# Performance work log

Measured on AMD Instinct MI355X. Metric: run time of the kernel, lower is better.

The kernel has to match this reference:

```python
import jax, jax.numpy as jnp
import numpy as np

D3D, D2D, DTEXT, DPROJ, SEQ_LEN = 256, 768, 3072, 3072, 256
B, S, T = 32, 256, 512


def setup_inputs() -> dict:
    key = jax.random.key(0)
    ks = jax.random.split(key, 9)
    s3 = 1.0 / np.sqrt(D3D)
    s2 = 1.0 / np.sqrt(D2D)
    sf = 1.0 / np.sqrt(DPROJ * 3)
    return {
        "feat_3d": jax.random.normal(ks[0], (B, D3D), jnp.float32),
        "feat_2d": jax.random.normal(ks[1], (B, S, D2D), jnp.float32),
        "feat_text": jax.random.normal(ks[2], (B, T, DTEXT), jnp.float32),
        "W3d": jax.random.uniform(ks[3], (DPROJ, D3D), jnp.float32, -s3, s3),
        "b3d": jax.random.uniform(ks[4], (DPROJ,), jnp.float32, -s3, s3),
        "W2d": jax.random.uniform(ks[5], (DPROJ, D2D), jnp.float32, -s2, s2),
        "b2d": jax.random.uniform(ks[6], (DPROJ,), jnp.float32, -s2, s2),
        "Wf": jax.random.uniform(ks[7], (DPROJ, DPROJ * 3), jnp.float32, -sf, sf),
        "bf": jax.random.uniform(ks[8], (DPROJ,), jnp.float32, -sf, sf),
    }


def reference(feat_3d, feat_2d, feat_text, W3d, b3d, W2d, b2d, Wf, bf):
    # Projections
    f3p = feat_3d @ W3d.T + b3d                      # [B, P]
    f2p = jnp.einsum("bsd,pd->bsp", feat_2d, W2d) + b2d  # [B, S, P]

    # Attention pooling of 2D slice features against global 3D feature
    scores_s = jnp.einsum("bsp,bp->bs", f2p, f3p)    # [B, S]
    w_s = jax.nn.softmax(scores_s, axis=1)
    pooled_2d = jnp.einsum("bs,bsp->bp", w_s, f2p)   # [B, P]

    # Attention pooling of text features against global 3D feature
    scores_t = jnp.einsum("btp,bp->bt", feat_text, f3p)  # [B, T]
    w_t = jax.nn.softmax(scores_t, axis=1)
    pooled_text = jnp.einsum("bt,btp->bp", w_t, feat_text)  # [B, P]

    # All seq_len rows of the original's concatenated input are identical,
    # so compute the fusion GEMM once per batch element and broadcast.
    fused_vec = jnp.concatenate([f3p, pooled_2d, pooled_text], axis=-1) @ Wf.T + bf  # [B, P]
    return jnp.broadcast_to(fused_vec[:, None, :], (fused_vec.shape[0], SEQ_LEN, fused_vec.shape[1]))
```

## Files before the change

### kernel.cpp

```cpp
#include <hip/hip_runtime.h>

#define NB 32
#define NS 256
#define NT 512
#define KD3 256
#define KD2 768
#define NP 3072
#define KFZ 9216

__device__ __forceinline__ float wave_red_sum(float v) {
#pragma unroll
  for (int o = 32; o; o >>= 1) v += __shfl_xor(v, o, 64);
  return v;
}
__device__ __forceinline__ float wave_red_max(float v) {
#pragma unroll
  for (int o = 32; o; o >>= 1) v = fmaxf(v, __shfl_xor(v, o, 64));
  return v;
}

__global__ __launch_bounds__(256) void k1_f3p(const float* __restrict__ f3d,
                                              const float* __restrict__ W3d,
                                              const float* __restrict__ b3d,
                                              float* __restrict__ c0, float* __restrict__ c1,
                                              float* __restrict__ c2, float* __restrict__ c3) {
  int b = blockIdx.x & 31, pc = blockIdx.x >> 5;
  __shared__ float4 xs[KD3 / 4];
  int tid = threadIdx.x;
  if (tid < KD3 / 4) xs[tid] = ((const float4*)(f3d + b * KD3))[tid];
  __syncthreads();
  int p = pc * 256 + tid;
  const float4* wrow = (const float4*)(W3d + (size_t)p * KD3);
  float acc = b3d[p];
#pragma unroll 8
  for (int i = 0; i < KD3 / 4; ++i) {
    float4 w = wrow[i], x = xs[i];
    acc = fmaf(w.x, x.x, acc); acc = fmaf(w.y, x.y, acc);
    acc = fmaf(w.z, x.z, acc); acc = fmaf(w.w, x.w, acc);
  }
  size_t o = (size_t)b * KFZ + p;
  c0[o] = acc; c1[o] = 0.f; c2[o] = 0.f; c3[o] = 0.f;
}

__global__ __launch_bounds__(256, 2) void kT_text(const float* __restrict__ ftx,
                                                  const float* __restrict__ c0,
                                                  float* __restrict__ Pt,
                                                  float* __restrict__ ml) {
  int b = blockIdx.x & 31, tch = blockIdx.x >> 5;
  __shared__ float4 f4[NP / 4];
  int tid = threadIdx.x;
#pragma unroll
  for (int i = 0; i < 3; ++i)
    f4[tid + 256 * i] = ((const float4*)(c0 + (size_t)b * KFZ))[tid + 256 * i];
  __syncthreads();
  int wave = tid >> 6, lane = tid & 63;
  int t0 = tch * 32 + wave * 8;
  const float4* rbase = (const float4*)(ftx + ((size_t)(b * NT + t0)) * NP);
  float4 xa[12], xb[12];
#pragma unroll
  for (int j = 0; j < 12; ++j) xa[j] = rbase[lane + 64 * j];
  float m = -3.0e38f, l = 0.f;
  float4 acc[12];
#pragma unroll
  for (int j = 0; j < 12; ++j) acc[j] = make_float4(0.f, 0.f, 0.f, 0.f);
#pragma unroll
  for (int r = 0; r < 8; ++r) {
    float4* cur = (r & 1) ? xb : xa;
    float4* nxt = (r & 1) ? xa : xb;
    if (r < 7) {
      const float4* rn = rbase + (size_t)(r + 1) * (NP / 4);
#pragma unroll
      for (int j = 0; j < 12; ++j) nxt[j] = rn[lane + 64 * j];
    }
    float sx = 0.f, sy = 0.f, sz = 0.f, sw = 0.f;
#pragma unroll
    for (int j = 0; j < 12; ++j) {
      float4 f = f4[lane + 64 * j];
      sx = fmaf(cur[j].x, f.x, sx); sy = fmaf(cur[j].y, f.y, sy);
      sz = fmaf(cur[j].z, f.z, sz); sw = fmaf(cur[j].w, f.w, sw);
    }
    float s = (sx + sy) + (sz + sw);
    s = wave_red_sum(s);
    float mn = fmaxf(m, s);
    float al = __expf(m - mn);
    float e = __expf(s - mn);
    l = fmaf(l, al, e);
#pragma unroll
    for (int j = 0; j < 12; ++j) {
      acc[j].x = fmaf(acc[j].x, al, e * cur[j].x);
      acc[j].y = fmaf(acc[j].y, al, e * cur[j].y);
      acc[j].z = fmaf(acc[j].z, al, e * cur[j].z);
      acc[j].w = fmaf(acc[j].w, al, e * cur[j].w);
    }
    m = mn;
  }
  int c = tch * 4 + wave;
  float4* Pr = (float4*)(Pt + (size_t)(c * NB + b) * NP);
#pragma unroll
  for (int j = 0; j < 12; ++j) Pr[lane + 64 * j] = acc[j];
  if (lane == 0) { ml[(c * NB + b) * 2] = m; ml[(c * NB + b) * 2 + 1] = l; }
}

__global__ __launch_bounds__(256) void k2_gpart(const float* __restrict__ W2d,
                                                const float* __restrict__ c0,
                                                float* __restrict__ g_part) {
  int dc = blockIdx.x % 3, kc = blockIdx.x / 3;
  __shared__ float xs[NB * 96];
  int tid = threadIdx.x;
  int p0 = kc * 96;
  for (int i = tid; i < NB * 96; i += 256) {
    int bb = i / 96, pp = i - bb * 96;
    xs[i] = c0[(size_t)bb * KFZ + p0 + pp];
  }
  __syncthreads();
  int d = dc * 256 + tid;
  float acc[NB];
#pragma unroll
  for (int b = 0; b < NB; ++b) acc[b] = 0.f;
  for (int pp = 0; pp < 96; pp += 8) {
    float w[8];
#pragma unroll
    for (int u = 0; u < 8; ++u) w[u] = W2d[(size_t)(p0 + pp + u) * KD2 + d];
#pragma unroll
    for (int b = 0; b < NB; ++b) {
      float4 x0 = *(const float4*)&xs[b * 96 + pp];
      float4 x1 = *(const float4*)&xs[b * 96 + pp + 4];
      acc[b] = fmaf(w[0], x0.x, acc[b]); acc[b] = fmaf(w[1], x0.y, acc[b]);
      acc[b] = fmaf(w[2], x0.z, acc[b]); acc[b] = fmaf(w[3], x0.w, acc[b]);
      acc[b] = fmaf(w[4], x1.x, acc[b]); acc[b] = fmaf(w[5], x1.y, acc[b]);
      acc[b] = fmaf(w[6], x1.z, acc[b]); acc[b] = fmaf(w[7], x1.w, acc[b]);
    }
  }
#pragma unroll
  for (int b = 0; b < NB; ++b) g_part[(size_t)(kc * NB + b) * KD2 + d] = acc[b];
}

__global__ __launch_bounds__(256) void k3a_scores(const float* __restrict__ f2d,
                                                  const float* __restrict__ g_part,
                                                  float* __restrict__ sraw) {
  int b = blockIdx.x & 31, sc = blockIdx.x >> 5;
  __shared__ float4 g4[KD2 / 4];
  float* g = (float*)g4;
  int tid = threadIdx.x;
  for (int i = tid; i < KD2; i += 256) {
    float a = 0.f;
#pragma unroll 8
    for (int c = 0; c < 32; ++c) a += g_part[(size_t)(c * NB + b) * KD2 + i];
    g[i] = a;
  }
  __syncthreads();
  int wave = tid >> 6, lane = tid & 63;
#pragma unroll
  for (int grp = 0; grp < 2; ++grp) {
    int s0 = sc * 32 + wave * 8 + grp * 4;
    float4 x[4][3];
#pragma unroll
    for (int rr = 0; rr < 4; ++rr) {
      const float4* row = (const float4*)(f2d + ((size_t)b * NS + s0 + rr) * KD2);
#pragma unroll
      for (int j = 0; j < 3; ++j) x[rr][j] = row[lane + 64 * j];
    }
#pragma unroll
    for (int rr = 0; rr < 4; ++rr) {
      float acc = 0.f;
#pragma unroll
      for (int j = 0; j < 3; ++j) {
        float4 f = g4[lane + 64 * j];
        acc = fmaf(x[rr][j].x, f.x, acc); acc = fmaf(x[rr][j].y, f.y, acc);
        acc = fmaf(x[rr][j].z, f.z, acc); acc = fmaf(x[rr][j].w, f.w, acc);
      }
      acc = wave_red_sum(acc);
      if (lane == 0) sraw[b * NS + s0 + rr] = acc;
    }
  }
}

__global__ __launch_bounds__(256) void kComb(const float* __restrict__ Pt,
                                             const float* __restrict__ ml,
                                             float* __restrict__ c0, float* __restrict__ c1,
                                             float* __restrict__ c2, float* __restrict__ c3) {
  int b = blockIdx.x & 31, pc = blockIdx.x >> 5;
  __shared__ float sm[128];
  int tid = threadIdx.x;
  if (tid < 64) {
    sm[tid] = ml[(tid * NB + b) * 2];
    sm[64 + tid] = ml[(tid * NB + b) * 2 + 1];
  }
  __syncthreads();
  float M = -3.0e38f;
#pragma unroll 8
  for (int c = 0; c < 64; ++c) M = fmaxf(M, sm[c]);
  float denom = 0.f;
#pragma unroll 8
  for (int c = 0; c < 64; ++c) denom += __expf(sm[c] - M) * sm[64 + c];
  float inv = 1.f / denom;
  int p4 = pc * 1024 + tid * 4;
  float4 a = make_float4(0.f, 0.f, 0.f, 0.f);
#pragma unroll 2
  for (int cg = 0; cg < 8; ++cg) {
    float4 v[8];
#pragma unroll
    for (int u = 0; u < 8; ++u)
      v[u] = *(const float4*)&Pt[(size_t)((cg * 8 + u) * NB + b) * NP + p4];
#pragma unroll
    for (int u = 0; u < 8; ++u) {
      float w = __expf(sm[cg * 8 + u] - M);
      a.x = fmaf(w, v[u].x, a.x); a.y = fmaf(w, v[u].y, a.y);
      a.z = fmaf(w, v[u].z, a.z); a.w = fmaf(w, v[u].w, a.w);
    }
  }
  a.x *= inv; a.y *= inv; a.z *= inv; a.w *= inv;
  size_t o = (size_t)b * KFZ + 2 * NP + p4;
  float4 z = make_float4(0.f, 0.f, 0.f, 0.f);
  *(float4*)&c0[o] = a;
  *(float4*)&c1[o] = z; *(float4*)&c2[o] = z; *(float4*)&c3[o] = z;
}

__global__ __launch_bounds__(256) void k3c_sm(const float* __restrict__ f2d,
                                              const float* __restrict__ sraw,
                                              float* __restrict__ p2f) {
  int b = blockIdx.x & 31;
  int r = blockIdx.x >> 5;
  int dc = r % 3, sc = r / 3;
  __shared__ float pr[NS];
  __shared__ float red[8];
  int tid = threadIdx.x;
  int wave = tid >> 6, lane = tid & 63;
  float v = sraw[b * NS + tid];
  float mx = wave_red_max(v);
  if (lane == 0) red[wave] = mx;
  __syncthreads();
  float M = fmaxf(fmaxf(red[0], red[1]), fmaxf(red[2], red[3]));
  float e = __expf(v - M);
  pr[tid] = e;
  float smv = wave_red_sum(e);
  if (lane == 0) red[4 + wave] = smv;
  __syncthreads();
  float inv = 1.f / (red[4] + red[5] + red[6] + red[7]);
  int d = dc * 256 + tid;
  float acc = 0.f;
  const float* base = f2d + ((size_t)b * NS + sc * 64) * KD2 + d;
#pragma unroll 2
  for (int sg = 0; sg < 8; ++sg) {
    float xv[8];
#pragma unroll
    for (int u = 0; u < 8; ++u) xv[u] = base[(size_t)(sg * 8 + u) * KD2];
#pragma unroll
    for (int u = 0; u < 8; ++u) acc = fmaf(pr[sc * 64 + sg * 8 + u], xv[u], acc);
  }
  p2f[(size_t)(sc * NB + b) * KD2 + d] = acc * inv;
}

__global__ __launch_bounds__(256) void k5_pool2d(const float* __restrict__ W2d,
                                                 const float* __restrict__ b2d,
                                                 const float* __restrict__ p2f,
                                                 float* __restrict__ c0, float* __restrict__ c1,
                                                 float* __restrict__ c2, float* __restrict__ c3) {
  int pb = blockIdx.x >> 2, ks = blockIdx.x & 3;
  __shared__ __align__(16) float wt[64 * 68];
  __shared__ __align__(16) float xt[32 * 68];
  int tid = threadIdx.x;
  int tp = tid & 31, tb = tid >> 5;
  float acc[2][4];
#pragma unroll
  for (int i = 0; i < 2; ++i)
#pragma unroll
    for (int j = 0; j < 4; ++j) acc[i][j] = 0.f;
  for (int dk = 0; dk < 3; ++dk) {
    int d0 = ks * 192 + dk * 64;
#pragma unroll
    for (int it = 0; it < 4; ++it) {
      int idx = tid + it * 256;
      int row = idx >> 4, c4 = (idx & 15) * 4;
      *(float4*)&wt[row * 68 + c4] =
          *(const float4*)&W2d[(size_t)(pb * 64 + row) * KD2 + d0 + c4];
    }
#pragma unroll
    for (int it = 0; it < 2; ++it) {
      int idx = tid + it * 256;
      int row = idx >> 4, c4 = (idx & 15) * 4;
      float4 a = *(const float4*)&p2f[(size_t)row * KD2 + d0 + c4];
      float4 q1 = *(const float4*)&p2f[(size_t)(NB + row) * KD2 + d0 + c4];
      float4 q2 = *(const float4*)&p2f[(size_t)(2 * NB + row) * KD2 + d0 + c4];
      float4 q3 = *(const float4*)&p2f[(size_t)(3 * NB + row) * KD2 + d0 + c4];
      a.x += q1.x + q2.x + q3.x; a.y += q1.y + q2.y + q3.y;
      a.z += q1.z + q2.z + q3.z; a.w += q1.w + q2.w + q3.w;
      *(float4*)&xt[row * 68 + c4] = a;
    }
    __syncthreads();
#pragma unroll 4
    for (int kk = 0; kk < 64; kk += 4) {
      float4 wv[2], xv[4];
#pragma unroll
      for (int i = 0; i < 2; ++i) wv[i] = *(const float4*)&wt[(tp + 32 * i) * 68 + kk];
#pragma unroll
      for (int j = 0; j < 4; ++j) xv[j] = *(const float4*)&xt[(tb + 8 * j) * 68 + kk];
#pragma unroll
      for (int i = 0; i < 2; ++i)
#pragma unroll
        for (int j = 0; j < 4; ++j) {
          acc[i][j] = fmaf(wv[i].x, xv[j].x, acc[i][j]);
          acc[i][j] = fmaf(wv[i].y, xv[j].y, acc[i][j]);
          acc[i][j] = fmaf(wv[i].z, xv[j].z, acc[i][j]);
          acc[i][j] = fmaf(wv[i].w, xv[j].w, acc[i][j]);
        }
    }
    __syncthreads();
  }
  float* dst = (ks == 0) ? c0 : (ks == 1) ? c1 : (ks == 2) ? c2 : c3;
#pragma unroll
  for (int i = 0; i < 2; ++i) {
    int p = pb * 64 + tp + 32 * i;
    float bias = (ks == 0) ? b2d[p] : 0.f;
#pragma unroll
    for (int j = 0; j < 4; ++j)
      dst[(size_t)(tb + 8 * j) * KFZ + NP + p] = acc[i][j] + bias;
  }
}

__global__ __launch_bounds__(256) void k_csum(float* __restrict__ c0,
                                              const float* __restrict__ c1,
                                              const float* __restrict__ c2,
                                              const float* __restrict__ c3) {
  int i = blockIdx.x * 256 + threadIdx.x;
  float4 a = ((float4*)c0)[i];
  float4 v1 = ((const float4*)c1)[i];
  float4 v2 = ((const float4*)c2)[i];
  float4 v3 = ((const float4*)c3)[i];
  a.x += v1.x + v2.x + v3.x; a.y += v1.y + v2.y + v3.y;
  a.z += v1.z + v2.z + v3.z; a.w += v1.w + v2.w + v3.w;
  ((float4*)c0)[i] = a;
}

__global__ __launch_bounds__(256, 1) void k6_fused(const float* __restrict__ Wf,
                                                   const float* __restrict__ c0,
                                                   float* __restrict__ fpart) {
  int pb = blockIdx.x & 3, kc = blockIdx.x >> 2;
  __shared__ float4 wt[2][4 * 768];
  __shared__ float4 xt[2][128];
  int tid = threadIdx.x;
  int wave = tid >> 6, lane = tid & 63;
  int p0g = pb * 768;
  int k00 = kc * 144;

  float acc[12][8];
#pragma unroll
  for (int i = 0; i < 12; ++i)
#pragma unroll
    for (int j = 0; j < 8; ++j) acc[i][j] = 0.f;

  float4 st[12];
  float4 xst;
  int xb = tid & 31, xk = tid >> 5;

  auto LOADS = [&](int t) {
    int k0 = k00 + t * 16;
#pragma unroll
    for (int it = 0; it < 12; ++it)
      st[it] = *(const float4*)&Wf[(size_t)(p0g + it * 64 + lane) * KFZ + k0 + wave * 4];
    if (tid < 128)
      xst = *(const float4*)&c0[(size_t)xb * KFZ + k0 + xk * 4];
  };
  auto WRITES = [&](int buf) {
#pragma unroll
    for (int it = 0; it < 12; ++it) wt[buf][wave * 768 + it * 64 + lane] = st[it];
    if (tid < 128) xt[buf][tid] = xst;
  };

  LOADS(0);
  WRITES(0);
  __syncthreads();
  for (int t = 0; t < 9; ++t) {
    int buf = t & 1;
    if (t < 8) LOADS(t + 1);
#pragma unroll
    for (int s = 0; s < 4; ++s) {
      float4 xv[8];
#pragma unroll
      for (int j = 0; j < 8; ++j) xv[j] = xt[buf][s * 32 + wave * 8 + j];
#pragma unroll
      for (int i = 0; i < 12; ++i) {
        float4 wv = wt[buf][s * 768 + i * 64 + lane];
#pragma unroll
        for (int j = 0; j < 8; ++j) {
          acc[i][j] = fmaf(wv.x, xv[j].x, acc[i][j]);
          acc[i][j] = fmaf(wv.y, xv[j].y, acc[i][j]);
          acc[i][j] = fmaf(wv.z, xv[j].z, acc[i][j]);
          acc[i][j] = fmaf(wv.w, xv[j].w, acc[i][j]);
        }
      }
    }
    if (t < 8) {
      WRITES(buf ^ 1);
      __syncthreads();
    }
  }
  float* fb = fpart + (size_t)(kc * NB + wave * 8) * NP + p0g + lane;
#pragma unroll
  for (int j = 0; j < 8; ++j)
#pragma unroll
    for (int i = 0; i < 12; ++i)
      fb[(size_t)j * NP + i * 64] = acc[i][j];
}

__global__ __launch_bounds__(256) void k7_bcast(const float* __restrict__ fpart,
                                                const float* __restrict__ bfv,
                                                float* __restrict__ out) {
  int b = blockIdx.x & 31;
  int pc = blockIdx.x >> 5;
  int tid = threadIdx.x;
  int p4 = pc * 1024 + 4 * tid;
  float4 v = *(const float4*)&bfv[p4];
#pragma unroll 8
  for (int c = 0; c < 64; ++c) {
    float4 a = *(const float4*)&fpart[(size_t)(c * NB + b) * NP + p4];
    v.x += a.x; v.y += a.y; v.z += a.z; v.w += a.w;
  }
  float* obase = out + (size_t)b * NS * NP + p4;
#pragma unroll 4
  for (int s = 0; s < NS; ++s)
    *(float4*)(obase + (size_t)s * NP) = v;
}

extern "C" void kernel_launch(void* const* d_in, const int* in_sizes, int n_in,
                              void* d_out, int out_size, void* d_ws, size_t ws_size,
                              hipStream_t stream) {
  const float* f3d = (const float*)d_in[0];
  const float* f2d = (const float*)d_in[1];
  const float* ftx = (const float*)d_in[2];
  const float* W3d = (const float*)d_in[3];
  const float* b3d = (const float*)d_in[4];
  const float* W2d = (const float*)d_in[5];
  const float* b2d = (const float*)d_in[6];
  const float* Wf  = (const float*)d_in[7];
  const float* bfv = (const float*)d_in[8];
  float* out = (float*)d_out;
  float* ws = (float*)d_ws;

  float* c0     = ws;
  float* c1     = ws + 294912;
  float* c2     = ws + 589824;
  float* c3     = ws + 884736;
  float* g_part = ws + 1179648;
  float* sraw   = ws + 1966080;
  float* p2f    = ws + 1974272;
  float* ml     = ws + 2072576;
  float* Pt     = ws + 2076672;
  float* fpart  = ws + 8368128;

  k1_f3p<<<384, 256, 0, stream>>>(f3d, W3d, b3d, c0, c1, c2, c3);
  kT_text<<<512, 256, 0, stream>>>(ftx, c0, Pt, ml);
  k2_gpart<<<96, 256, 0, stream>>>(W2d, c0, g_part);
  k3a_scores<<<256, 256, 0, stream>>>(f2d, g_part, sraw);
  kComb<<<96, 256, 0, stream>>>(Pt, ml, c0, c1, c2, c3);
  k3c_sm<<<384, 256, 0, stream>>>(f2d, sraw, p2f);
  k5_pool2d<<<192, 256, 0, stream>>>(W2d, b2d, p2f, c0, c1, c2, c3);
  k_csum<<<288, 256, 0, stream>>>(c0, c1, c2, c3);
  k6_fused<<<256, 256, 0, stream>>>(Wf, c0, fpart);
  k7_bcast<<<96, 256, 0, stream>>>(fpart, bfv, out);
}
```

Before: 610.5 us.

## Split split-K reduction and widen broadcast grid; coalesce Wf tile loads

The fusion GEMM's Wf tile load now has each thread read four contiguous float4s of one row, so a thread fetches 64 contiguous bytes instead of one strided float4 per row slice. The 64-way split-K reduction moves into a separate kernel that folds groups of 8 partials, and the broadcast kernel grows from 96 to 768 blocks, each writing 32 sequence rows. The aim is more parallelism for the output write and partial reduction, which were limited to 96 blocks. The cost is an extra launch and an intermediate buffer that reuses the Pt workspace region.

```diff
diff --git a/kernel.cpp b/kernel.cpp
--- a/kernel.cpp
+++ b/kernel.cpp
@@ -349,21 +349,27 @@
 #pragma unroll
     for (int j = 0; j < 8; ++j) acc[i][j] = 0.f;
 
-  float4 st[12];
+  float4 st[3][4];
   float4 xst;
   int xb = tid & 31, xk = tid >> 5;
 
   auto LOADS = [&](int t) {
     int k0 = k00 + t * 16;
 #pragma unroll
-    for (int it = 0; it < 12; ++it)
-      st[it] = *(const float4*)&Wf[(size_t)(p0g + it * 64 + lane) * KFZ + k0 + wave * 4];
+    for (int r = 0; r < 3; ++r) {
+      const float4* src = (const float4*)&Wf[(size_t)(p0g + r * 256 + tid) * KFZ + k0];
+#pragma unroll
+      for (int kk = 0; kk < 4; ++kk) st[r][kk] = src[kk];
+    }
     if (tid < 128)
       xst = *(const float4*)&c0[(size_t)xb * KFZ + k0 + xk * 4];
   };
   auto WRITES = [&](int buf) {
 #pragma unroll
-    for (int it = 0; it < 12; ++it) wt[buf][wave * 768 + it * 64 + lane] = st[it];
+    for (int r = 0; r < 3; ++r)
+#pragma unroll
+      for (int kk = 0; kk < 4; ++kk)
+        wt[buf][kk * 768 + r * 256 + tid] = st[r][kk];
     if (tid < 128) xt[buf][tid] = xst;
   };
 
@@ -403,23 +409,43 @@
       fb[(size_t)j * NP + i * 64] = acc[i][j];
 }
 
-__global__ __launch_bounds__(256) void k7_bcast(const float* __restrict__ fpart,
+__global__ __launch_bounds__(256) void k7a_red(const float* __restrict__ fpart,
+                                               float* __restrict__ fpart2) {
+  int b = blockIdx.x & 31, g = blockIdx.x >> 5;
+  int tid = threadIdx.x;
+#pragma unroll
+  for (int i = 0; i < 3; ++i) {
+    int p4 = i * 256 + tid;
+    float4 a = make_float4(0.f, 0.f, 0.f, 0.f);
+#pragma unroll
+    for (int c = 0; c < 8; ++c) {
+      float4 v = ((const float4*)&fpart[(size_t)((g * 8 + c) * NB + b) * NP])[p4];
+      a.x += v.x; a.y += v.y; a.z += v.z; a.w += v.w;
+    }
+    ((float4*)&fpart2[(size_t)(g * NB + b) * NP])[p4] = a;
+  }
+}
+
+__global__ __launch_bounds__(256) void k7_bcast(const float* __restrict__ fpart2,
                                                 const float* __restrict__ bfv,
                                                 float* __restrict__ out) {
   int b = blockIdx.x & 31;
-  int pc = blockIdx.x >> 5;
+  int r = blockIdx.x >> 5;
+  int pc = r % 3, sc = r / 3;
   int tid = threadIdx.x;
   int p4 = pc * 1024 + 4 * tid;
   float4 v = *(const float4*)&bfv[p4];
-#pragma unroll 8
-  for (int c = 0; c < 64; ++c) {
-    float4 a = *(const float4*)&fpart[(size_t)(c * NB + b) * NP + p4];
+#pragma unroll
+  for (int c = 0; c < 8; ++c) {
+    float4 a = *(const float4*)&fpart2[(size_t)(c * NB + b) * NP + p4];
     v.x += a.x; v.y += a.y; v.z += a.z; v.w += a.w;
   }
   float* obase = out + (size_t)b * NS * NP + p4;
 #pragma unroll 4
-  for (int s = 0; s < NS; ++s)
+  for (int ss = 0; ss < 32; ++ss) {
+    int s = sc * 32 + ss;
     *(float4*)(obase + (size_t)s * NP) = v;
+  }
 }
 
 extern "C" void kernel_launch(void* const* d_in, const int* in_sizes, int n_in,
@@ -447,6 +473,7 @@
   float* ml     = ws + 2072576;
   float* Pt     = ws + 2076672;
   float* fpart  = ws + 8368128;
+  float* fpart2 = ws + 2076672;
 
   k1_f3p<<<384, 256, 0, stream>>>(f3d, W3d, b3d, c0, c1, c2, c3);
   kT_text<<<512, 256, 0, stream>>>(ftx, c0, Pt, ml);
@@ -457,5 +484,6 @@
   k5_pool2d<<<192, 256, 0, stream>>>(W2d, b2d, p2f, c0, c1, c2, c3);
   k_csum<<<288, 256, 0, stream>>>(c0, c1, c2, c3);
   k6_fused<<<256, 256, 0, stream>>>(Wf, c0, fpart);
-  k7_bcast<<<96, 256, 0, stream>>>(fpart, bfv, out);
-}
+  k7a_red<<<256, 256, 0, stream>>>(fpart, fpart2);
+  k7_bcast<<<768, 256, 0, stream>>>(fpart2, bfv, out);
+}
```

Result: faster. 576.6 us (-5.5%).
